# Optimization experiments

Measured on AMD Instinct MI355X. Metric: run time of the kernel, lower is better.

The kernel has to match this reference:

```python
import jax, jax.numpy as jnp
import numpy as np
import math

EMBED_DIM = 64
NUM_HEADS = 4
HEAD_DIM = EMBED_DIM // NUM_HEADS
TGT = 64
SRC = 64
BSZ = 128


def setup_inputs() -> dict:
    key = jax.random.key(0)
    ks = jax.random.split(key, 8)
    x = jax.random.normal(ks[0], (TGT, BSZ, EMBED_DIM), dtype=jnp.float32)
    relation = jax.random.normal(ks[1], (TGT, SRC, BSZ, EMBED_DIM), dtype=jnp.float32)
    in_proj_weight = jax.random.normal(ks[2], (3 * EMBED_DIM, EMBED_DIM), dtype=jnp.float32) * 0.02
    in_proj_bias = jnp.zeros((3 * EMBED_DIM,), dtype=jnp.float32)
    rel_weight = jax.random.normal(ks[3], (2 * EMBED_DIM, EMBED_DIM), dtype=jnp.float32) * 0.02
    rel_bias = jnp.zeros((2 * EMBED_DIM,), dtype=jnp.float32)
    out_weight = jax.random.normal(ks[4], (EMBED_DIM, EMBED_DIM), dtype=jnp.float32) * 0.02
    out_bias = jnp.zeros((EMBED_DIM,), dtype=jnp.float32)
    return {
        'query': x, 'key': x, 'value': x, 'relation': relation,
        'in_proj_weight': in_proj_weight, 'in_proj_bias': in_proj_bias,
        'rel_weight': rel_weight, 'rel_bias': rel_bias,
        'out_weight': out_weight, 'out_bias': out_bias,
    }


def reference(query, key, value, relation, in_proj_weight, in_proj_bias,
              rel_weight, rel_bias, out_weight, out_bias):
    E, H, hd = EMBED_DIM, NUM_HEADS, HEAD_DIM
    t, b, _ = query.shape
    s = key.shape[0]
    scaling = hd ** (-0.5)
    # qkv projections (slices of the fused in_proj weight, as in _in_proj)
    q = query @ in_proj_weight[:E].T + in_proj_bias[:E]
    k = key @ in_proj_weight[E:2 * E].T + in_proj_bias[E:2 * E]
    v = value @ in_proj_weight[2 * E:].T + in_proj_bias[2 * E:]
    q = q.reshape(t, b * H, hd)
    k = k.reshape(s, b * H, hd)
    v = v.reshape(s, b * H, hd)
    # relation projection -> ra, rb, each [t, s, b*H, hd], then transpose(0,1)
    rel = relation @ rel_weight.T + rel_bias  # [t, s, b, 2E]
    ra = rel[..., :E].reshape(t, s, b * H, hd).swapaxes(0, 1)  # [s, t, bH, hd]
    rb = rel[..., E:].reshape(t, s, b * H, hd).swapaxes(0, 1)
    # q[i,j] = q[i] + ra_t[i,j]; requires t == s (broadcast as in torch)
    qp = (q[:, None] + ra) * scaling            # [t, s, bH, hd]
    kp = k[None, :] + rb                        # [t, s, bH, hd]
    attn_weights = jnp.einsum('ijbn,ijbn->ijb', qp, kp) * (1.0 / math.sqrt(hd))
    attn_weights = jax.nn.softmax(attn_weights, axis=1)
    attn = jnp.einsum('ijb,jbn->bin', attn_weights, v)  # [bH, t, hd]
    attn = attn.swapaxes(0, 1).reshape(t, b, E)
    out = attn @ out_weight.T + out_bias
    return out
```

## Files before the change

### kernel.cpp

```cpp
#include <hip/hip_runtime.h>
#include <hip/hip_bf16.h>

#define T_ 64
#define S_ 64
#define B_ 128
#define E_ 64
#define H_ 4

typedef float f32x4 __attribute__((ext_vector_type(4)));
typedef short bf16x8 __attribute__((ext_vector_type(8)));

static __device__ __forceinline__ short f2b(float f) {
    union { __hip_bfloat16 h; short s; } u;
    u.h = __float2bfloat16(f);
    return u.s;
}

__global__ __launch_bounds__(256) void k_qkv(
    const float* __restrict__ qin, const float* __restrict__ kin,
    const float* __restrict__ vin, const float* __restrict__ W,
    const float* __restrict__ bias, float* __restrict__ qkv)
{
    __shared__ float xs[3][32 * 68];
    __shared__ float WTs[64 * 68];
    const int tid = threadIdx.x;
    const int row0 = blockIdx.x * 32;

    #pragma unroll
    for (int l = 0; l < 6; ++l) {
        int f4 = l * 256 + tid;
        int src = f4 >> 9, rem = f4 & 511;
        int r = rem >> 4, e0 = (rem & 15) << 2;
        const float* xin = (src == 0) ? qin : (src == 1 ? kin : vin);
        float4 xv = reinterpret_cast<const float4*>(xin)[(size_t)(row0 + r) * 16 + (e0 >> 2)];
        float* dst = &xs[src][r * 68];
        dst[e0] = xv.x; dst[e0 + 1] = xv.y; dst[e0 + 2] = xv.z; dst[e0 + 3] = xv.w;
    }

    const int rq = tid >> 5, og = tid & 31;
    const int r0 = rq * 4, op0 = og * 2;

    for (int seg = 0; seg < 3; ++seg) {
        __syncthreads();
        #pragma unroll
        for (int l = 0; l < 4; ++l) {
            int f4 = l * 256 + tid;
            int o = f4 >> 4, e0 = (f4 & 15) << 2;
            float4 wv = reinterpret_cast<const float4*>(W)[(size_t)(seg * 64 + o) * 16 + (e0 >> 2)];
            WTs[(e0 + 0) * 68 + o] = wv.x; WTs[(e0 + 1) * 68 + o] = wv.y;
            WTs[(e0 + 2) * 68 + o] = wv.z; WTs[(e0 + 3) * 68 + o] = wv.w;
        }
        __syncthreads();

        float acc[4][2];
        #pragma unroll
        for (int rr = 0; rr < 4; ++rr) {
            acc[rr][0] = bias[seg * 64 + op0];
            acc[rr][1] = bias[seg * 64 + op0 + 1];
        }
        const float* xsrc = xs[seg];
        #pragma unroll 4
        for (int e = 0; e < 64; ++e) {
            float w0 = WTs[e * 68 + op0];
            float w1 = WTs[e * 68 + op0 + 1];
            #pragma unroll
            for (int rr = 0; rr < 4; ++rr) {
                float xv = xsrc[(r0 + rr) * 68 + e];
                acc[rr][0] += xv * w0;
                acc[rr][1] += xv * w1;
            }
        }
        #pragma unroll
        for (int rr = 0; rr < 4; ++rr) {
            float2 ov = make_float2(acc[rr][0], acc[rr][1]);
            reinterpret_cast<float2*>(
                &qkv[((size_t)seg * T_ * B_ + row0 + r0 + rr) * E_ + op0])[0] = ov;
        }
    }
}

__global__ __launch_bounds__(256, 3) void k_logits_mfma(
    const float* __restrict__ rel, const float* __restrict__ relW,
    const float* __restrict__ relBias, const float* __restrict__ qkv,
    float* __restrict__ logits)
{
    __shared__ char Bs[16384];

    const int tid = threadIdx.x;
    const int w   = tid >> 6;
    const int l   = tid & 63;
    const int c   = l & 15;
    const int rq  = l >> 4;
    const int g   = blockIdx.x & 1;
    const int j   = (blockIdx.x >> 1) & 63;
    const int i   = blockIdx.x >> 7;
    const int btile = g * 4 + w;

    const int arow = ((btile * 16 + c) * E_) + rq * 8;
    float4 a0, a1, a2, a3;
    {
        const float* ab = rel + ((size_t)j * S_ + i) * (size_t)(B_ * E_) + arow;
        a0 = *(const float4*)(ab);
        a1 = *(const float4*)(ab + 4);
        a2 = *(const float4*)(ab + 32);
        a3 = *(const float4*)(ab + 36);
    }

    #pragma unroll
    for (int li = 0; li < 8; ++li) {
        int f4 = li * 256 + tid;
        int o = f4 >> 4, e4 = f4 & 15;
        float4 wv = reinterpret_cast<const float4*>(relW)[f4];
        ushort4 bv;
        bv.x = (ushort)f2b(wv.x); bv.y = (ushort)f2b(wv.y);
        bv.z = (ushort)f2b(wv.z); bv.w = (ushort)f2b(wv.w);
        int ot = o >> 4, cc = o & 15;
        int ks = e4 >> 3, rqb = (e4 & 7) >> 1, half = e4 & 1;
        int dest = (ot * 2 + ks) * 1024 + (rqb * 16 + cc) * 16 + half * 8;
        *reinterpret_cast<ushort4*>(Bs + dest) = bv;
    }

    float qpre[4][4], bbv[4];
    {
        const float* qrow = qkv + (size_t)i * (B_ * E_);
        #pragma unroll
        for (int h = 0; h < 4; ++h) {
            float ba = relBias[h * 16 + c];
            bbv[h] = relBias[64 + h * 16 + c];
            #pragma unroll
            for (int r = 0; r < 4; ++r) {
                int b = btile * 16 + rq * 4 + r;
                qpre[h][r] = qrow[b * E_ + h * 16 + c] + ba;
            }
        }
    }
    __syncthreads();

    float kvv[4][4];
    {
        const float* krow = qkv + ((size_t)(T_ * B_) + (size_t)j * B_ + btile * 16 + rq * 4) * E_;
        #pragma unroll
        for (int h = 0; h < 4; ++h)
            #pragma unroll
            for (int r = 0; r < 4; ++r)
                kvv[h][r] = krow[r * E_ + h * 16 + c];
    }

    bf16x8 af0, af1;
    {
        bf16x8 a;
        a[0] = f2b(a0.x); a[1] = f2b(a0.y); a[2] = f2b(a0.z); a[3] = f2b(a0.w);
        a[4] = f2b(a1.x); a[5] = f2b(a1.y); a[6] = f2b(a1.z); a[7] = f2b(a1.w);
        af0 = a;
        a[0] = f2b(a2.x); a[1] = f2b(a2.y); a[2] = f2b(a2.z); a[3] = f2b(a2.w);
        a[4] = f2b(a3.x); a[5] = f2b(a3.y); a[6] = f2b(a3.z); a[7] = f2b(a3.w);
        af1 = a;
    }

    f32x4 acc[8];
    #pragma unroll
    for (int ot = 0; ot < 8; ++ot) acc[ot] = (f32x4){0.f, 0.f, 0.f, 0.f};
    #pragma unroll
    for (int ot = 0; ot < 8; ++ot) {
        bf16x8 b0 = *(const bf16x8*)(Bs + (ot * 2 + 0) * 1024 + l * 16);
        bf16x8 b1 = *(const bf16x8*)(Bs + (ot * 2 + 1) * 1024 + l * 16);
        acc[ot] = __builtin_amdgcn_mfma_f32_16x16x32_bf16(af0, b0, acc[ot], 0, 0, 0);
        acc[ot] = __builtin_amdgcn_mfma_f32_16x16x32_bf16(af1, b1, acc[ot], 0, 0, 0);
    }

    float v[16];
    #pragma unroll
    for (int h = 0; h < 4; ++h)
        #pragma unroll
        for (int r = 0; r < 4; ++r)
            v[h * 4 + r] = (qpre[h][r] + acc[h][r]) *
                           (kvv[h][r] + bbv[h] + acc[4 + h][r]);
    #pragma unroll
    for (int k = 0; k < 8; ++k) {
        float x = (c & 1) ? v[2 * k + 1] : v[2 * k];
        float y = (c & 1) ? v[2 * k] : v[2 * k + 1];
        v[k] = x + __shfl_xor(y, 1);
    }
    #pragma unroll
    for (int k = 0; k < 4; ++k) {
        float x = (c & 2) ? v[2 * k + 1] : v[2 * k];
        float y = (c & 2) ? v[2 * k] : v[2 * k + 1];
        v[k] = x + __shfl_xor(y, 2);
    }
    #pragma unroll
    for (int k = 0; k < 2; ++k) {
        float x = (c & 4) ? v[2 * k + 1] : v[2 * k];
        float y = (c & 4) ? v[2 * k] : v[2 * k + 1];
        v[k] = x + __shfl_xor(y, 4);
    }
    float outv;
    {
        float x = (c & 8) ? v[1] : v[0];
        float y = (c & 8) ? v[0] : v[1];
        outv = (x + __shfl_xor(y, 8)) * 0.0625f;
    }

    {
        const int off = btile * 64 + rq * 16 + (c & 3) * 4 + (c >> 2);
        logits[((size_t)i * S_ + j) * (B_ * H_) + off] = outv;
    }
}

__global__ __launch_bounds__(256) void k_attn(
    const float* __restrict__ logits, const float* __restrict__ qkv,
    const float* __restrict__ Wout, const float* __restrict__ bout,
    float* __restrict__ out)
{
    __shared__ float wsm[4][H_][S_];
    __shared__ float ap[4][68];
    const int tid = threadIdx.x;
    const int i = blockIdx.x >> 5;
    const int bq = blockIdx.x & 31;
    const int w = tid >> 6, l = tid & 63;
    const int b = bq * 4 + w;

    const int h = l >> 4, sub = l & 15;
    const float* lg = logits + (size_t)i * S_ * (B_ * H_) + b * H_ + h;
    float v0 = lg[(size_t)(sub +  0) * (B_ * H_)];
    float v1 = lg[(size_t)(sub + 16) * (B_ * H_)];
    float v2 = lg[(size_t)(sub + 32) * (B_ * H_)];
    float v3 = lg[(size_t)(sub + 48) * (B_ * H_)];
    float m = fmaxf(fmaxf(v0, v1), fmaxf(v2, v3));
    #pragma unroll
    for (int d = 1; d < 16; d <<= 1) m = fmaxf(m, __shfl_xor(m, d));
    float e0 = expf(v0 - m), e1 = expf(v1 - m), e2 = expf(v2 - m), e3 = expf(v3 - m);
    float ss = e0 + e1 + e2 + e3;
    #pragma unroll
    for (int d = 1; d < 16; d <<= 1) ss += __shfl_xor(ss, d);
    float inv = 1.0f / ss;
    wsm[w][h][sub] = e0 * inv;
    wsm[w][h][sub + 16] = e1 * inv;
    wsm[w][h][sub + 32] = e2 * inv;
    wsm[w][h][sub + 48] = e3 * inv;
    __syncthreads();

    const float* vbase = qkv + (size_t)2 * T_ * B_ * E_ + (size_t)b * E_;
    const float* wrow = &wsm[w][l >> 4][0];
    float acc = 0.f;
    #pragma unroll 4
    for (int j = 0; j < S_; ++j) acc += wrow[j] * vbase[(size_t)j * B_ * E_ + l];
    ap[w][l] = acc;
    __syncthreads();

    const float* wo = Wout + l * E_;
    const float* apw = ap[w];
    float oacc = bout[l];
    #pragma unroll 4
    for (int e = 0; e < E_; ++e) oacc += apw[e] * wo[e];
    out[((size_t)i * B_ + b) * E_ + l] = oacc;
}

extern "C" void kernel_launch(void* const* d_in, const int* in_sizes, int n_in,
                              void* d_out, int out_size, void* d_ws, size_t ws_size,
                              hipStream_t stream)
{
    const float* qin = (const float*)d_in[0];
    const float* kin = (const float*)d_in[1];
    const float* vin = (const float*)d_in[2];
    const float* rel = (const float*)d_in[3];
    const float* ipw = (const float*)d_in[4];
    const float* ipb = (const float*)d_in[5];
    const float* rw  = (const float*)d_in[6];
    const float* rb  = (const float*)d_in[7];
    const float* ow  = (const float*)d_in[8];
    const float* obias = (const float*)d_in[9];

    float* qkv = (float*)d_ws;
    float* logits = qkv + 3 * T_ * B_ * E_;
    float* out = (float*)d_out;

    k_qkv<<<dim3(256), dim3(256), 0, stream>>>(qin, kin, vin, ipw, ipb, qkv);
    k_logits_mfma<<<dim3(8192), dim3(256), 0, stream>>>(rel, rw, rb, qkv, logits);
    k_attn<<<dim3(2048), dim3(256), 0, stream>>>(logits, qkv, ow, obias, out);
}
```

Before: 78.36 us.

## Precompute bf16 relation weights once and load MFMA B-fragments directly from global

The relation-weight fp32-to-bf16 conversion and swizzle moves out of each of the 8192 logits blocks into one extra block of the QKV kernel, which writes a pre-laid-out bf16 buffer to workspace. The logits kernel then loads MFMA B fragments straight into registers from global memory (L2-resident), dropping the shared-memory staging and barrier and raising the occupancy hint to 4. The attention kernel now stages logits through shared memory with coalesced float4 loads instead of strided scalar loads. The cost is more registers held for the B fragments, plus dependence on the extra block finishing before the next launch, which stream ordering guarantees.

```diff
diff --git a/kernel.cpp b/kernel.cpp
--- a/kernel.cpp
+++ b/kernel.cpp
@@ -19,11 +19,30 @@
 __global__ __launch_bounds__(256) void k_qkv(
     const float* __restrict__ qin, const float* __restrict__ kin,
     const float* __restrict__ vin, const float* __restrict__ W,
-    const float* __restrict__ bias, float* __restrict__ qkv)
-{
+    const float* __restrict__ bias, float* __restrict__ qkv,
+    const float* __restrict__ relW, ushort* __restrict__ wBf)
+{
+    const int tid = threadIdx.x;
+
+    if (blockIdx.x == 256) {
+        #pragma unroll
+        for (int li = 0; li < 8; ++li) {
+            int f4 = li * 256 + tid;
+            int o = f4 >> 4, e4 = f4 & 15;
+            float4 wv = reinterpret_cast<const float4*>(relW)[f4];
+            ushort4 bv;
+            bv.x = (ushort)f2b(wv.x); bv.y = (ushort)f2b(wv.y);
+            bv.z = (ushort)f2b(wv.z); bv.w = (ushort)f2b(wv.w);
+            int ot = o >> 4, cc = o & 15;
+            int ks = e4 >> 3, rqb = (e4 & 7) >> 1, half = e4 & 1;
+            int dest = (ot * 2 + ks) * 512 + (rqb * 16 + cc) * 8 + half * 4;
+            *reinterpret_cast<ushort4*>(wBf + dest) = bv;
+        }
+        return;
+    }
+
     __shared__ float xs[3][32 * 68];
     __shared__ float WTs[64 * 68];
-    const int tid = threadIdx.x;
     const int row0 = blockIdx.x * 32;
 
     #pragma unroll
@@ -79,13 +98,11 @@
     }
 }
 
-__global__ __launch_bounds__(256, 3) void k_logits_mfma(
-    const float* __restrict__ rel, const float* __restrict__ relW,
+__global__ __launch_bounds__(256, 4) void k_logits_mfma(
+    const float* __restrict__ rel, const ushort* __restrict__ wBf,
     const float* __restrict__ relBias, const float* __restrict__ qkv,
     float* __restrict__ logits)
 {
-    __shared__ char Bs[16384];
-
     const int tid = threadIdx.x;
     const int w   = tid >> 6;
     const int l   = tid & 63;
@@ -106,23 +123,37 @@
         a3 = *(const float4*)(ab + 36);
     }
 
-    #pragma unroll
-    for (int li = 0; li < 8; ++li) {
-        int f4 = li * 256 + tid;
-        int o = f4 >> 4, e4 = f4 & 15;
-        float4 wv = reinterpret_cast<const float4*>(relW)[f4];
-        ushort4 bv;
-        bv.x = (ushort)f2b(wv.x); bv.y = (ushort)f2b(wv.y);
-        bv.z = (ushort)f2b(wv.z); bv.w = (ushort)f2b(wv.w);
-        int ot = o >> 4, cc = o & 15;
-        int ks = e4 >> 3, rqb = (e4 & 7) >> 1, half = e4 & 1;
-        int dest = (ot * 2 + ks) * 1024 + (rqb * 16 + cc) * 16 + half * 8;
-        *reinterpret_cast<ushort4*>(Bs + dest) = bv;
-    }
-
-    float qpre[4][4], bbv[4];
+    bf16x8 bfr[8][2];
+    #pragma unroll
+    for (int ot = 0; ot < 8; ++ot)
+        #pragma unroll
+        for (int ks = 0; ks < 2; ++ks)
+            bfr[ot][ks] = *(const bf16x8*)(wBf + (ot * 2 + ks) * 512 + l * 8);
+
+    bf16x8 af0, af1;
+    {
+        bf16x8 a;
+        a[0] = f2b(a0.x); a[1] = f2b(a0.y); a[2] = f2b(a0.z); a[3] = f2b(a0.w);
+        a[4] = f2b(a1.x); a[5] = f2b(a1.y); a[6] = f2b(a1.z); a[7] = f2b(a1.w);
+        af0 = a;
+        a[0] = f2b(a2.x); a[1] = f2b(a2.y); a[2] = f2b(a2.z); a[3] = f2b(a2.w);
+        a[4] = f2b(a3.x); a[5] = f2b(a3.y); a[6] = f2b(a3.z); a[7] = f2b(a3.w);
+        af1 = a;
+    }
+
+    f32x4 acc[8];
+    #pragma unroll
+    for (int ot = 0; ot < 8; ++ot) acc[ot] = (f32x4){0.f, 0.f, 0.f, 0.f};
+    #pragma unroll
+    for (int ot = 0; ot < 8; ++ot) {
+        acc[ot] = __builtin_amdgcn_mfma_f32_16x16x32_bf16(af0, bfr[ot][0], acc[ot], 0, 0, 0);
+        acc[ot] = __builtin_amdgcn_mfma_f32_16x16x32_bf16(af1, bfr[ot][1], acc[ot], 0, 0, 0);
+    }
+
+    float qpre[4][4], bbv[4], kvv[4][4];
     {
         const float* qrow = qkv + (size_t)i * (B_ * E_);
+        const float* krow = qkv + ((size_t)(T_ * B_) + (size_t)j * B_ + btile * 16 + rq * 4) * E_;
         #pragma unroll
         for (int h = 0; h < 4; ++h) {
             float ba = relBias[h * 16 + c];
@@ -131,41 +162,9 @@
             for (int r = 0; r < 4; ++r) {
                 int b = btile * 16 + rq * 4 + r;
                 qpre[h][r] = qrow[b * E_ + h * 16 + c] + ba;
+                kvv[h][r] = krow[r * E_ + h * 16 + c];
             }
         }
-    }
-    __syncthreads();
-
-    float kvv[4][4];
-    {
-        const float* krow = qkv + ((size_t)(T_ * B_) + (size_t)j * B_ + btile * 16 + rq * 4) * E_;
-        #pragma unroll
-        for (int h = 0; h < 4; ++h)
-            #pragma unroll
-            for (int r = 0; r < 4; ++r)
-                kvv[h][r] = krow[r * E_ + h * 16 + c];
-    }
-
-    bf16x8 af0, af1;
-    {
-        bf16x8 a;
-        a[0] = f2b(a0.x); a[1] = f2b(a0.y); a[2] = f2b(a0.z); a[3] = f2b(a0.w);
-        a[4] = f2b(a1.x); a[5] = f2b(a1.y); a[6] = f2b(a1.z); a[7] = f2b(a1.w);
-        af0 = a;
-        a[0] = f2b(a2.x); a[1] = f2b(a2.y); a[2] = f2b(a2.z); a[3] = f2b(a2.w);
-        a[4] = f2b(a3.x); a[5] = f2b(a3.y); a[6] = f2b(a3.z); a[7] = f2b(a3.w);
-        af1 = a;
-    }
-
-    f32x4 acc[8];
-    #pragma unroll
-    for (int ot = 0; ot < 8; ++ot) acc[ot] = (f32x4){0.f, 0.f, 0.f, 0.f};
-    #pragma unroll
-    for (int ot = 0; ot < 8; ++ot) {
-        bf16x8 b0 = *(const bf16x8*)(Bs + (ot * 2 + 0) * 1024 + l * 16);
-        bf16x8 b1 = *(const bf16x8*)(Bs + (ot * 2 + 1) * 1024 + l * 16);
-        acc[ot] = __builtin_amdgcn_mfma_f32_16x16x32_bf16(af0, b0, acc[ot], 0, 0, 0);
-        acc[ot] = __builtin_amdgcn_mfma_f32_16x16x32_bf16(af1, b1, acc[ot], 0, 0, 0);
     }
 
     float v[16];
@@ -211,6 +210,7 @@
     const float* __restrict__ Wout, const float* __restrict__ bout,
     float* __restrict__ out)
 {
+    __shared__ float trans[64][20];
     __shared__ float wsm[4][H_][S_];
     __shared__ float ap[4][68];
     const int tid = threadIdx.x;
@@ -219,12 +219,19 @@
     const int w = tid >> 6, l = tid & 63;
     const int b = bq * 4 + w;
 
+    {
+        const int jj = tid >> 2, q = tid & 3;
+        float4 lv = *(const float4*)(logits + ((size_t)i * S_ + jj) * (B_ * H_) + bq * 16 + q * 4);
+        *reinterpret_cast<float4*>(&trans[jj][q * 4]) = lv;
+    }
+    __syncthreads();
+
     const int h = l >> 4, sub = l & 15;
-    const float* lg = logits + (size_t)i * S_ * (B_ * H_) + b * H_ + h;
-    float v0 = lg[(size_t)(sub +  0) * (B_ * H_)];
-    float v1 = lg[(size_t)(sub + 16) * (B_ * H_)];
-    float v2 = lg[(size_t)(sub + 32) * (B_ * H_)];
-    float v3 = lg[(size_t)(sub + 48) * (B_ * H_)];
+    const int col = w * 4 + h;
+    float v0 = trans[sub][col];
+    float v1 = trans[sub + 16][col];
+    float v2 = trans[sub + 32][col];
+    float v3 = trans[sub + 48][col];
     float m = fmaxf(fmaxf(v0, v1), fmaxf(v2, v3));
     #pragma unroll
     for (int d = 1; d < 16; d <<= 1) m = fmaxf(m, __shfl_xor(m, d));
@@ -272,9 +279,11 @@
 
     float* qkv = (float*)d_ws;
     float* logits = qkv + 3 * T_ * B_ * E_;
+    ushort* wBf = (ushort*)(logits + (size_t)T_ * S_ * B_ * H_);
+
     float* out = (float*)d_out;
 
-    k_qkv<<<dim3(256), dim3(256), 0, stream>>>(qin, kin, vin, ipw, ipb, qkv);
-    k_logits_mfma<<<dim3(8192), dim3(256), 0, stream>>>(rel, rw, rb, qkv, logits);
+    k_qkv<<<dim3(257), dim3(256), 0, stream>>>(qin, kin, vin, ipw, ipb, qkv, rw, wBf);
+    k_logits_mfma<<<dim3(8192), dim3(256), 0, stream>>>(rel, wBf, rb, qkv, logits);
     k_attn<<<dim3(2048), dim3(256), 0, stream>>>(logits, qkv, ow, obias, out);
 }
```

New measurement: 83.63 us. 1.07x slower.
